# Performance work log

Measured on AMD Instinct MI355X. Metric: run time of the kernel, lower is better.

Reference implementation:

```python
import jax, jax.numpy as jnp
import numpy as np

D = 512      # d_model
H = 8        # n_head
L = 6        # n_layers
DFF = 2048   # d_inner
V = 10000    # vocab
NPOS = 2048
B, T = 8, 1023
S = 1024     # encoder length


def sinusoid_table(n_position, d_hid):
    pos = np.arange(n_position)[:, None].astype(np.float64)
    i = np.arange(d_hid)[None, :]
    angle = pos / np.power(10000.0, 2 * (i // 2) / d_hid)
    tab = np.zeros((n_position, d_hid))
    tab[:, 0::2] = np.sin(angle[:, 0::2])
    tab[:, 1::2] = np.cos(angle[:, 1::2])
    return jnp.asarray(tab, jnp.float32)


def layer_norm(x, g, b, eps=1e-6):
    m = x.mean(-1, keepdims=True)
    v = x.var(-1, keepdims=True)
    return (x - m) / jnp.sqrt(v + eps) * g + b


def mha(x, kv, wq, wk, wv, wo, g, b, mask):
    # x: [B,Lq,D], kv: [B,Lk,D], mask: [B,Lq|1,Lk] int or None
    Bq, Lq, _ = x.shape
    Lk = kv.shape[1]
    dk = D // H
    q = (x @ wq).reshape(Bq, Lq, H, dk).transpose(0, 2, 1, 3)   # bhqd
    k = (kv @ wk).reshape(Bq, Lk, H, dk).transpose(0, 2, 1, 3)  # bhkd
    v = (kv @ wv).reshape(Bq, Lk, H, dk).transpose(0, 2, 1, 3)
    scores = jnp.einsum('bhqd,bhkd->bhqk', q, k) / jnp.sqrt(jnp.asarray(dk, x.dtype))
    if mask is not None:
        scores = jnp.where(mask[:, None, :, :] == 0, jnp.asarray(-1e9, x.dtype), scores)
    a = jax.nn.softmax(scores, axis=-1)
    o = jnp.einsum('bhqk,bhkd->bhqd', a, v).transpose(0, 2, 1, 3).reshape(Bq, Lq, D)
    o = o @ wo + x  # residual
    return layer_norm(o, g, b)


def ffn(x, w1, b1, w2, b2, g, b):
    h = jax.nn.relu(x @ w1 + b1)
    return layer_norm(h @ w2 + b2 + x, g, b)


def setup_inputs() -> dict:
    key = jax.random.key(0)
    ks = iter(jax.random.split(key, 64))
    sc = 0.02
    inp = {}
    inp['trg_seq'] = jax.random.randint(next(ks), (B, T), 0, V, dtype=jnp.int32)
    # causal mask over decoder length T+1 (1 = attend)
    T1 = T + 1
    inp['trg_mask'] = jnp.tril(jnp.ones((T1, T1), jnp.int32))[None].repeat(B, axis=0)
    inp['enc_output'] = jax.random.normal(next(ks), (B, S, D), jnp.float32)
    inp['src_mask'] = jnp.ones((B, 1, S), jnp.int32)
    inp['emb'] = jax.random.normal(next(ks), (V, D), jnp.float32) * sc
    inp['ln0_g'] = jnp.ones((D,), jnp.float32)
    inp['ln0_b'] = jnp.zeros((D,), jnp.float32)
    for nm in ['wq_s', 'wk_s', 'wv_s', 'wo_s', 'wq_c', 'wk_c', 'wv_c', 'wo_c']:
        inp[nm] = jax.random.normal(next(ks), (L, D, D), jnp.float32) * sc
    for nm in ['ln1_g', 'ln2_g', 'ln3_g']:
        inp[nm] = jnp.ones((L, D), jnp.float32)
    for nm in ['ln1_b', 'ln2_b', 'ln3_b']:
        inp[nm] = jnp.zeros((L, D), jnp.float32)
    inp['w1'] = jax.random.normal(next(ks), (L, D, DFF), jnp.float32) * sc
    inp['b1'] = jnp.zeros((L, DFF), jnp.float32)
    inp['w2'] = jax.random.normal(next(ks), (L, DFF, D), jnp.float32) * sc
    inp['b2'] = jnp.zeros((L, D), jnp.float32)
    return inp


def reference(trg_seq, trg_mask, enc_output, src_mask, emb, ln0_g, ln0_b,
              wq_s, wk_s, wv_s, wo_s, ln1_g, ln1_b,
              wq_c, wk_c, wv_c, wo_c, ln2_g, ln2_b,
              w1, b1, w2, b2, ln3_g, ln3_b):
    Bq, Tq = trg_seq.shape
    tok = emb[trg_seq]                                         # [B,T,D]
    x = jnp.concatenate([jnp.zeros((Bq, 1, D), tok.dtype), tok], axis=1)  # [B,T+1,D]
    x = x + sinusoid_table(NPOS, D)[None, :Tq + 1]
    x = layer_norm(x, ln0_g, ln0_b)
    for l in range(L):
        x = mha(x, x, wq_s[l], wk_s[l], wv_s[l], wo_s[l], ln1_g[l], ln1_b[l], trg_mask)
        x = mha(x, enc_output, wq_c[l], wk_c[l], wv_c[l], wo_c[l], ln2_g[l], ln2_b[l], src_mask)
        x = ffn(x, w1[l], b1[l], w2[l], b2[l], ln3_g[l], ln3_b[l])
    return x
```

## Files before the change

kernel.cpp:

```cpp
#include <hip/hip_runtime.h>
#include <stdint.h>


typedef unsigned short u16;
typedef float floatx4 __attribute__((ext_vector_type(4)));
typedef short short8 __attribute__((ext_vector_type(8)));

__device__ __forceinline__ float b2f(u16 u) {
    union { unsigned int i; float f; } c; c.i = ((unsigned int)u) << 16; return c.f;
}
__device__ __forceinline__ u16 f2b(float f) {
    union { float f; unsigned int i; } c; c.f = f;
    return (u16)((c.i + 0x7FFFu + ((c.i >> 16) & 1u)) >> 16);
}
__device__ __forceinline__ float ldf(const void* p, size_t i, bool is32) {
    return is32 ? ((const float*)p)[i] : b2f(((const u16*)p)[i]);
}
__device__ __forceinline__ void async16(u16* lds, const u16* g) {
    __builtin_amdgcn_global_load_lds(
        (const __attribute__((address_space(1))) unsigned int*)g,
        (__attribute__((address_space(3))) unsigned int*)lds, 16, 0, 0);
}
__device__ __forceinline__ void xcd_remap(int gx, int gy, int& bx, int& by) {
    const int fid = bx + gx * by;
    const int xcd = fid & 7;
    const int i = fid >> 3;
    bx = i % gx;
    by = xcd * (gy >> 3) + i / gx;
}

__global__ __launch_bounds__(256)
void conv_bf16_kernel(const void* __restrict__ src, u16* __restrict__ dst,
                      const u16* __restrict__ probe)
{
    const bool is32 = (probe[0] == 0);
    const size_t off = ((size_t)blockIdx.x * 256 + threadIdx.x) * 4;
    u16 o[4];
    if (is32) {
        float4 f = *(const float4*)((const float*)src + off);
        o[0] = f2b(f.x); o[1] = f2b(f.y); o[2] = f2b(f.z); o[3] = f2b(f.w);
    } else {
        uint2 vv = *(const uint2*)((const u16*)src + off);
        const u16* pv = (const u16*)&vv;
        o[0] = pv[0]; o[1] = pv[1]; o[2] = pv[2]; o[3] = pv[3];
    }
    *(uint2*)&dst[off] = *(uint2*)o;
}

__global__ __launch_bounds__(256)
void transpose_layer_kernel(const void* __restrict__ wq_s, const void* __restrict__ wk_s,
                            const void* __restrict__ wv_s, const void* __restrict__ wo_s,
                            const void* __restrict__ wq_c, const void* __restrict__ wk_c,
                            const void* __restrict__ wv_c, const void* __restrict__ wo_c,
                            const void* __restrict__ w1,   const void* __restrict__ w2,
                            u16* __restrict__ wT, const u16* __restrict__ probe,
                            size_t loff2, size_t loff1)
{
    __shared__ u16 tile[32][33];
    const bool is32 = (probe[0] == 0);
    const int bid = blockIdx.x;
    const int tid = threadIdx.x;
    const void* src; u16* dst; int C, R, tr, tc; size_t loff;
    if (bid < 2048) {
        const int mat = bid >> 8, t = bid & 255;
        R = 512; C = 512; tr = t >> 4; tc = t & 15; loff = loff2;
        const void* tbl[8] = {wq_s, wk_s, wv_s, wo_s, wq_c, wk_c, wv_c, wo_c};
        src = tbl[mat]; dst = wT + (size_t)mat * 262144;
    } else if (bid < 3072) {
        const int t = bid - 2048;
        R = 512; C = 2048; tr = t >> 6; tc = t & 63; loff = loff1;
        src = w1; dst = wT + 2097152;
    } else {
        const int t = bid - 3072;
        R = 2048; C = 512; tr = t >> 4; tc = t & 15; loff = loff1;
        src = w2; dst = wT + 3145728;
    }
    const int r = tid >> 3, c0 = (tid & 7) * 4;
    const size_t off = loff + (size_t)(tr * 32 + r) * C + tc * 32 + c0;
    u16 vals[4];
    if (is32) {
        float4 f = *(const float4*)((const float*)src + off);
        vals[0] = f2b(f.x); vals[1] = f2b(f.y); vals[2] = f2b(f.z); vals[3] = f2b(f.w);
    } else {
        uint2 vv = *(const uint2*)((const u16*)src + off);
        const u16* pv = (const u16*)&vv;
        vals[0] = pv[0]; vals[1] = pv[1]; vals[2] = pv[2]; vals[3] = pv[3];
    }
#pragma unroll
    for (int j = 0; j < 4; j++) tile[r][c0 + j] = vals[j];
    __syncthreads();
    uint2 ov; u16* po = (u16*)&ov;
#pragma unroll
    for (int j = 0; j < 4; j++) po[j] = tile[c0 + j][r];
    *(uint2*)&dst[(size_t)(tc * 32 + r) * R + tr * 32 + c0] = ov;
}

template<int EPI>
__global__ __launch_bounds__(512)
void gemm256(const u16* __restrict__ A, const u16* __restrict__ Bt,
             const void* __restrict__ bias, size_t boff,
             u16* __restrict__ outb, u16* __restrict__ out1, u16* __restrict__ out2,
             const u16* __restrict__ probe, int M, int N, int K)
{
    __shared__ u16 As[2][256 * 64];
    __shared__ u16 Bs[2][256 * 64];
    const int tid = threadIdx.x;
    const int lane = tid & 63;
    const int quad = lane >> 4, cl = lane & 15;
    const int wave = tid >> 6;
    const int wm2 = (wave >> 2) * 128;
    const int wn2 = (wave & 3) * 64;
    int bx = blockIdx.x, by = blockIdx.y;
    xcd_remap(gridDim.x, gridDim.y, bx, by);
    const int m0 = by * 256, n0 = bx * 256;

    floatx4 acc[8][4];
#pragma unroll
    for (int i = 0; i < 8; i++)
#pragma unroll
        for (int j = 0; j < 4; j++)
#pragma unroll
            for (int r = 0; r < 4; r++) acc[i][j][r] = 0.0f;

    const int lrow = lane >> 3;
    const int lcol = ((lane & 7) ^ lrow) * 8;
    const u16* gA = &A [(size_t)(m0 + wave * 8 + lrow) * K + lcol];
    const u16* gB = &Bt[(size_t)(n0 + wave * 8 + lrow) * K + lcol];

    auto stage = [&](int bsel, int k0) {
#pragma unroll
        for (int s = 0; s < 4; s++)
            async16(&As[bsel][(s * 64 + wave * 8) * 64], gA + (size_t)s * 64 * K + k0);
#pragma unroll
        for (int s = 0; s < 4; s++)
            async16(&Bs[bsel][(s * 64 + wave * 8) * 64], gB + (size_t)s * 64 * K + k0);
    };

    const int nkt = K >> 6;
    stage(0, 0);
    stage(1, 64);

    const int c7 = cl & 7;
    for (int t = 0; t < nkt; ++t) {
        const int cur = t & 1;
        if (t == nkt - 1) asm volatile("s_waitcnt vmcnt(0)" ::: "memory");
        else              asm volatile("s_waitcnt vmcnt(8)" ::: "memory");
        __builtin_amdgcn_sched_barrier(0);
        __builtin_amdgcn_s_barrier();

        const u16* Ac = As[cur];
        const u16* Bc = Bs[cur];
#pragma unroll
        for (int kk = 0; kk < 2; kk++) {
            const int gsw = ((kk * 4 + quad) ^ c7) * 8;
            short8 af[8], bf[4];
#pragma unroll
            for (int mi = 0; mi < 8; mi++)
                af[mi] = *(const short8*)&Ac[(wm2 + mi * 16 + cl) * 64 + gsw];
#pragma unroll
            for (int ni = 0; ni < 4; ni++)
                bf[ni] = *(const short8*)&Bc[(wn2 + ni * 16 + cl) * 64 + gsw];
#pragma unroll
            for (int mi = 0; mi < 8; mi++)
#pragma unroll
                for (int ni = 0; ni < 4; ni++)
                    acc[mi][ni] = __builtin_amdgcn_mfma_f32_16x16x32_bf16(af[mi], bf[ni], acc[mi][ni], 0, 0, 0);
        }
        __builtin_amdgcn_s_barrier();
        __builtin_amdgcn_sched_barrier(0);
        if (t + 2 < nkt) stage(cur, (t + 2) * 64);
    }

    const bool is32 = (probe[0] == 0);
#pragma unroll
    for (int mi = 0; mi < 8; mi++) {
#pragma unroll
        for (int ni = 0; ni < 4; ni++) {
            const int col = n0 + wn2 + ni * 16 + cl;
            const float bv = ldf(bias, boff + col, is32);
#pragma unroll
            for (int r = 0; r < 4; r++) {
                const int row = m0 + wm2 + mi * 16 + quad * 4 + r;
                float v = acc[mi][ni][r] + bv;
                v = fmaxf(v, 0.0f);
                outb[(size_t)row * N + col] = f2b(v);
            }
        }
    }
}

template<int EPI>
__global__ __launch_bounds__(256)
void gemm_bf16(const u16* __restrict__ A, const u16* __restrict__ Bt,
               const void* __restrict__ bias, size_t boff, float* __restrict__ resid,
               u16* __restrict__ outb, u16* __restrict__ out1, u16* __restrict__ out2,
               const u16* __restrict__ probe, int M, int N, int K)
{
    __shared__ u16 As[3][128 * 32];
    __shared__ u16 Bs[3][128 * 32];
    const int tid = threadIdx.x;
    const int lane = tid & 63;
    const int quad = lane >> 4, cl = lane & 15;
    const int wave = tid >> 6;
    const int wm = (wave >> 1) * 64, wn = (wave & 1) * 64;
    int bx = blockIdx.x, by = blockIdx.y;
    xcd_remap(gridDim.x, gridDim.y, bx, by);
    const int m0 = by * 128, n0 = bx * 128;

    const u16* Ause = A;
    if (EPI == 4) {
        const u16* A2 = (const u16*)bias;
        if (A2 != nullptr && n0 >= 512) Ause = A2;
    }

    floatx4 acc[4][4];
#pragma unroll
    for (int i = 0; i < 4; i++)
#pragma unroll
        for (int j = 0; j < 4; j++)
#pragma unroll
            for (int r = 0; r < 4; r++) acc[i][j][r] = 0.0f;

    const int srow = tid >> 2;
    const int scol = (((tid & 3) ^ ((srow >> 1) & 3))) * 8;
    const int rslot = (quad ^ ((cl >> 1) & 3)) * 8;
    const int Ksub = K / gridDim.z;
    const int kbeg = blockIdx.z * Ksub, kend = kbeg + Ksub;
    const int nsteps = (kend - kbeg) >> 5;

    const u16* ga0 = &Ause[(size_t)(m0 + srow) * K + scol];
    const u16* ga1 = &Ause[(size_t)(m0 + 64 + srow) * K + scol];
    const u16* gb0 = &Bt[(size_t)(n0 + srow) * K + scol];
    const u16* gb1 = &Bt[(size_t)(n0 + 64 + srow) * K + scol];

    auto stage = [&](int bsel, int kk) {
        async16(&As[bsel][wave * 512],        ga0 + kk);
        async16(&As[bsel][2048 + wave * 512], ga1 + kk);
        async16(&Bs[bsel][wave * 512],        gb0 + kk);
        async16(&Bs[bsel][2048 + wave * 512], gb1 + kk);
    };

    stage(0, kbeg);
    if (nsteps > 1) stage(1, kbeg + 32);

    for (int t = 0; t < nsteps; ++t) {
        const int cur = t % 3;
        if (t + 2 < nsteps) stage((t + 2) % 3, kbeg + (t + 2) * 32);
        const int rem = nsteps - 1 - t;
        if (rem >= 2)      asm volatile("s_waitcnt vmcnt(8)" ::: "memory");
        else if (rem == 1) asm volatile("s_waitcnt vmcnt(4)" ::: "memory");
        else               asm volatile("s_waitcnt vmcnt(0)" ::: "memory");
        __builtin_amdgcn_sched_barrier(0);
        __builtin_amdgcn_s_barrier();

        const u16* Ac = As[cur];
        const u16* Bc = Bs[cur];
        short8 af[4], bfr[4];
#pragma unroll
        for (int mi = 0; mi < 4; mi++) af[mi]  = *(const short8*)&Ac[(wm + mi * 16 + cl) * 32 + rslot];
#pragma unroll
        for (int ni = 0; ni < 4; ni++) bfr[ni] = *(const short8*)&Bc[(wn + ni * 16 + cl) * 32 + rslot];
#pragma unroll
        for (int mi = 0; mi < 4; mi++)
#pragma unroll
            for (int ni = 0; ni < 4; ni++)
                acc[mi][ni] = __builtin_amdgcn_mfma_f32_16x16x32_bf16(af[mi], bfr[ni], acc[mi][ni], 0, 0, 0);
        __builtin_amdgcn_s_barrier();
    }

    if (EPI == 4) {
        const int seg = n0 >> 9;
        const int cbase = (n0 & 511) + wn;
        if (seg < 2) {
            u16* dst = (seg == 0) ? outb : out1;
#pragma unroll
            for (int mi = 0; mi < 4; mi++)
#pragma unroll
                for (int ni = 0; ni < 4; ni++) {
                    const int c = cbase + ni * 16 + cl;
#pragma unroll
                    for (int r = 0; r < 4; r++)
                        dst[(size_t)(m0 + wm + mi * 16 + quad * 4 + r) * 512 + c] = f2b(acc[mi][ni][r]);
                }
        } else {
            u16* dst = out2;
#pragma unroll
            for (int mi = 0; mi < 4; mi++) {
                const int row0 = m0 + wm + mi * 16 + quad * 4;
                const int b8 = (row0 >> 10) * 8;
                const int key0 = row0 & 1023;
#pragma unroll
                for (int ni = 0; ni < 4; ni++) {
                    const int c = cbase + ni * 16 + cl;
                    u16 pk[4];
#pragma unroll
                    for (int r = 0; r < 4; r++) pk[r] = f2b(acc[mi][ni][r]);
                    const size_t vrow = (size_t)(b8 + (c >> 6)) * 64 + (c & 63);
                    *(uint2*)&dst[vrow * 1024 + key0] = *(uint2*)pk;
                }
            }
        }
        return;
    }

    bool is32 = false;
    if (EPI == 1 || EPI == 2 || EPI == 3) is32 = (probe[0] == 0);
    const bool addbias = (bias != nullptr) && (blockIdx.z == 0);
    float* pslice = (EPI == 3) ? resid + (size_t)blockIdx.z * M * N : resid;
#pragma unroll
    for (int mi = 0; mi < 4; mi++) {
#pragma unroll
        for (int ni = 0; ni < 4; ni++) {
            const int col = n0 + wn + ni * 16 + cl;
#pragma unroll
            for (int r = 0; r < 4; r++) {
                const int row = m0 + wm + mi * 16 + quad * 4 + r;
                float v = acc[mi][ni][r];
                if (EPI == 1) { v += ldf(bias, boff + col, is32); v = fmaxf(v, 0.0f); }
                if (EPI == 2) {
                    if (addbias) v += ldf(bias, boff + col, is32);
                    atomicAdd(&resid[(size_t)row * N + col], v);
                } else if (EPI == 3) {
                    if (addbias) v += ldf(bias, boff + col, is32);
                    pslice[(size_t)row * N + col] = v;
                } else {
                    outb[(size_t)row * N + col] = f2b(v);
                }
            }
        }
    }
}

template<int CAUSAL>
__global__ __launch_bounds__(512)
void attn_kernel(const u16* __restrict__ Q, const u16* __restrict__ Kb,
                 const u16* __restrict__ VT, u16* __restrict__ O)
{
    __shared__ u16 Kt[2][64][72];
    __shared__ u16 Vt[2][64][72];
    int qt = blockIdx.x, bh = blockIdx.y;
    xcd_remap(gridDim.x, gridDim.y, qt, bh);
    const int b = bh >> 3, h = bh & 7;
    const int tid = threadIdx.x;
    const int w = tid >> 6;
    const int lane = tid & 63;
    const int quad = lane >> 4, cl = lane & 15;

    const size_t qrow = (size_t)(b * 1024 + qt * 128 + w * 16 + cl) * 512 + h * 64;
    const short8 qf0 = *(const short8*)&Q[qrow + quad * 8];
    const short8 qf1 = *(const short8*)&Q[qrow + 32 + quad * 8];
    const int qg = qt * 128 + w * 16 + cl;

    float lsum = 0.0f;
    floatx4 oacc[4];
#pragma unroll
    for (int nb = 0; nb < 4; nb++)
#pragma unroll
        for (int r = 0; r < 4; r++) oacc[nb][r] = 0.0f;

    const int trow = tid >> 3, tcol = (tid & 7) * 8;
    const int tv = tid & 7;
    const int vm = (tv >> 2) * 32 + (tv & 1) * 16 + ((tv >> 1) & 1) * 4;
    const size_t kbase = (size_t)(b * 1024) * 512 + h * 64;
    const size_t vbase = (size_t)(bh * 64) * 1024;

    const int nkt = CAUSAL ? (2 * qt + 2) : 16;
    uint4 ka = *(const uint4*)&Kb[kbase + (size_t)trow * 512 + tcol];
    uint4 va = *(const uint4*)&VT[vbase + (size_t)trow * 1024 + tcol];

    for (int kt = 0; kt < nkt; kt++) {
        const int cur = kt & 1;
        asm volatile("s_waitcnt vmcnt(0)" ::: "memory");
        *(uint4*)&Kt[cur][trow][tcol]      = ka;
        *(uint2*)&Vt[cur][trow][vm]        = make_uint2(va.x, va.y);
        *(uint2*)&Vt[cur][trow][vm + 8]    = make_uint2(va.z, va.w);
        if (kt + 1 < nkt) {
            const int k1 = (kt + 1) * 64;
            ka = *(const uint4*)&Kb[kbase + (size_t)(k1 + trow) * 512 + tcol];
            va = *(const uint4*)&VT[vbase + (size_t)trow * 1024 + k1 + tcol];
        }
        asm volatile("s_waitcnt lgkmcnt(0)" ::: "memory");
        __builtin_amdgcn_sched_barrier(0);
        __builtin_amdgcn_s_barrier();
        __builtin_amdgcn_sched_barrier(0);

        const int k0 = kt * 64;
        floatx4 sacc[4];
#pragma unroll
        for (int kb2 = 0; kb2 < 4; kb2++)
#pragma unroll
            for (int r = 0; r < 4; r++) sacc[kb2][r] = 0.0f;
#pragma unroll
        for (int kb2 = 0; kb2 < 4; kb2++) {
            const short8 kf0 = *(const short8*)&Kt[cur][kb2 * 16 + cl][quad * 8];
            const short8 kf1 = *(const short8*)&Kt[cur][kb2 * 16 + cl][32 + quad * 8];
            sacc[kb2] = __builtin_amdgcn_mfma_f32_16x16x32_bf16(kf0, qf0, sacc[kb2], 0, 0, 0);
            sacc[kb2] = __builtin_amdgcn_mfma_f32_16x16x32_bf16(kf1, qf1, sacc[kb2], 0, 0, 0);
        }
        const bool need_mask = CAUSAL && (kt >= nkt - 2);
        float p[4][4];
#pragma unroll
        for (int kb2 = 0; kb2 < 4; kb2++) {
#pragma unroll
            for (int r = 0; r < 4; r++) {
                float e = __expf(sacc[kb2][r] * 0.125f);
                if (need_mask) {
                    const int key = k0 + kb2 * 16 + quad * 4 + r;
                    e = (key > qg) ? 0.0f : e;
                }
                p[kb2][r] = e;
                lsum += e;
            }
        }
        unsigned int pk[4][2];
#pragma unroll
        for (int kb2 = 0; kb2 < 4; kb2++) {
            asm("v_cvt_pk_bf16_f32 %0, %1, %2" : "=v"(pk[kb2][0]) : "v"(p[kb2][0]), "v"(p[kb2][1]));
            asm("v_cvt_pk_bf16_f32 %0, %1, %2" : "=v"(pk[kb2][1]) : "v"(p[kb2][2]), "v"(p[kb2][3]));
        }
#pragma unroll
        for (int c = 0; c < 2; c++) {
            union { short8 s8; unsigned int u[4]; } pa;
            pa.u[0] = pk[2 * c][0];     pa.u[1] = pk[2 * c][1];
            pa.u[2] = pk[2 * c + 1][0]; pa.u[3] = pk[2 * c + 1][1];
#pragma unroll
            for (int nb = 0; nb < 4; nb++) {
                const short8 vf = *(const short8*)&Vt[cur][nb * 16 + cl][c * 32 + quad * 8];
                oacc[nb] = __builtin_amdgcn_mfma_f32_16x16x32_bf16(pa.s8, vf, oacc[nb], 0, 0, 0);
            }
        }
    }
    lsum += __shfl_xor(lsum, 16, 64);
    lsum += __shfl_xor(lsum, 32, 64);
    float inv[4];
#pragma unroll
    for (int r = 0; r < 4; r++) inv[r] = 1.0f / __shfl(lsum, quad * 4 + r, 64);
#pragma unroll
    for (int nb = 0; nb < 4; nb++) {
#pragma unroll
        for (int r = 0; r < 4; r++) {
            const float v = oacc[nb][r] * inv[r];
            O[(size_t)(b * 1024 + qt * 128 + w * 16 + quad * 4 + r) * 512 + h * 64 + nb * 16 + cl] = f2b(v);
        }
    }
}

__device__ __forceinline__ float2 block_ln_512(float v0, float v1,
                                               float g0, float g1, float b0, float b1,
                                               int tid)
{
    __shared__ float red[8];
    float s = v0 + v1, sq = v0 * v0 + v1 * v1;
#pragma unroll
    for (int m = 1; m < 64; m <<= 1) { s += __shfl_xor(s, m, 64); sq += __shfl_xor(sq, m, 64); }
    const int wv = tid >> 6;
    if ((tid & 63) == 0) { red[wv * 2] = s; red[wv * 2 + 1] = sq; }
    __syncthreads();
    s  = red[0] + red[2] + red[4] + red[6];
    sq = red[1] + red[3] + red[5] + red[7];
    const float mean = s * (1.0f / 512.0f);
    const float var = sq * (1.0f / 512.0f) - mean * mean;
    const float rstd = rsqrtf(var + 1e-6f);
    return make_float2((v0 - mean) * rstd * g0 + b0, (v1 - mean) * rstd * g1 + b1);
}

__global__ __launch_bounds__(256)
void ln_kernel(float* __restrict__ xf, const void* __restrict__ g, const void* __restrict__ bb,
               size_t goff, const u16* __restrict__ probe,
               u16* __restrict__ xb, void* __restrict__ finalout,
               const float* __restrict__ p0, const float* __restrict__ p1)
{
    const bool is32 = (probe[0] == 0);
    const int row = blockIdx.x, tid = threadIdx.x;
    const int i = tid * 2;
    const size_t base = (size_t)row * 512;
    float2 v = *(const float2*)&xf[base + i];
    if (p0) {
        const float2 a = *(const float2*)&p0[base + i];
        v.x += a.x; v.y += a.y;
    }
    if (p1) {
        const float2 b = *(const float2*)&p1[base + i];
        v.x += b.x; v.y += b.y;
    }
    const float2 y = block_ln_512(v.x, v.y, ldf(g, goff + i, is32), ldf(g, goff + i + 1, is32),
                                  ldf(bb, goff + i, is32), ldf(bb, goff + i + 1, is32), tid);
    if (finalout) {
        if (is32) {
            *(float2*)&((float*)finalout)[base + i] = y;
        } else {
            u16* ob = (u16*)finalout;
            ob[base + i] = f2b(y.x); ob[base + i + 1] = f2b(y.y);
        }
    } else {
        *(float2*)&xf[base + i] = y;
        xb[base + i] = f2b(y.x); xb[base + i + 1] = f2b(y.y);
    }
}

__global__ __launch_bounds__(256)
void embed_ln_kernel(const int* __restrict__ trg_seq, const void* __restrict__ emb,
                     const void* __restrict__ g, const void* __restrict__ bb,
                     const u16* __restrict__ probe,
                     float* __restrict__ xf, u16* __restrict__ xb)
{
    const bool is32 = (probe[0] == 0);
    const int row = blockIdx.x;
    const int b = row >> 10, t = row & 1023;
    const int tid = threadIdx.x;
    const int tok = (t == 0) ? -1 : trg_seq[b * 1023 + t - 1];
    const int i = tid * 2;
    const float freq = __expf((float)i * (-9.210340371976184f / 512.0f));
    const float angle = (float)t * freq;
    float v0 = sinf(angle), v1 = cosf(angle);
    if (tok >= 0) {
        v0 += ldf(emb, (size_t)tok * 512 + i, is32);
        v1 += ldf(emb, (size_t)tok * 512 + i + 1, is32);
    }
    const float2 y = block_ln_512(v0, v1, ldf(g, i, is32), ldf(g, i + 1, is32),
                                  ldf(bb, i, is32), ldf(bb, i + 1, is32), tid);
    const size_t base = (size_t)row * 512;
    *(float2*)&xf[base + i] = y;
    xb[base + i] = f2b(y.x); xb[base + i + 1] = f2b(y.y);
}

extern "C" void kernel_launch(void* const* d_in, const int* in_sizes, int n_in,
                              void* d_out, int out_size, void* d_ws, size_t ws_size,
                              hipStream_t stream)
{
    const int* trg_seq = (const int*)d_in[0];
    const void* enc   = d_in[2];
    const void* emb   = d_in[4];
    const void* ln0_g = d_in[5];
    const void* ln0_b = d_in[6];
    const u16* probe  = (const u16*)d_in[5];

    char* ws = (char*)d_ws;
    float* xf   = (float*)(ws);
    u16*   xb   = (u16*)  (ws + (16u << 20));
    u16*   qb   = (u16*)  (ws + (24u << 20));
    u16*   kb   = (u16*)  (ws + (32u << 20));
    u16*   vt   = (u16*)  (ws + (40u << 20));
    u16*   ao   = (u16*)  (ws + (48u << 20));
    u16*   hb   = (u16*)  (ws + (24u << 20));
    u16*   wT   = (u16*)  (ws + (56u << 20));
    u16*   encb = (u16*)  (ws + (64u << 20));
    const bool bigws = ws_size >= (108ull << 20);
    float* p0 = (float*)(ws + (72u << 20));
    float* p1 = (float*)(ws + (88u << 20));
    const float* lp0 = bigws ? p0 : nullptr;
    const float* lp1 = bigws ? p1 : nullptr;

    const size_t E2 = 262144, E1 = 1048576;
    const dim3 gqkv(12, 64);
    const dim3 gffn1(8, 32);
    const dim3 gproj(4, 64);
    const dim3 gffn2(4, 64, 2);
    const dim3 gattn(8, 64);

    conv_bf16_kernel<<<4096, 256, 0, stream>>>(enc, encb, probe);
    embed_ln_kernel<<<8192, 256, 0, stream>>>(trg_seq, emb, ln0_g, ln0_b, probe, xf, xb);

    for (int l = 0; l < 6; l++) {
        transpose_layer_kernel<<<4096, 256, 0, stream>>>(
            d_in[7], d_in[8], d_in[9], d_in[10], d_in[11], d_in[12], d_in[13], d_in[14],
            d_in[21], d_in[23], wT, probe, (size_t)l * E2, (size_t)l * E1);

        gemm_bf16<4><<<gqkv, 256, 0, stream>>>(xb, wT, xb, 0, nullptr,
                                               qb, kb, vt, probe, 8192, 1536, 512);
        attn_kernel<1><<<gattn, 512, 0, stream>>>(qb, kb, vt, ao);
        if (bigws)
            gemm_bf16<3><<<gproj, 256, 0, stream>>>(ao, wT + 3 * E2, nullptr, 0, p0,
                                                    nullptr, nullptr, nullptr, probe, 8192, 512, 512);
        else
            gemm_bf16<2><<<gproj, 256, 0, stream>>>(ao, wT + 3 * E2, nullptr, 0, xf,
                                                    nullptr, nullptr, nullptr, probe, 8192, 512, 512);
        ln_kernel<<<8192, 256, 0, stream>>>(xf, d_in[15], d_in[18], (size_t)l * 512, probe, xb,
                                            nullptr, lp0, nullptr);

        gemm_bf16<4><<<gqkv, 256, 0, stream>>>(xb, wT + 4 * E2, encb, 0, nullptr,
                                               qb, kb, vt, probe, 8192, 1536, 512);
        attn_kernel<0><<<gattn, 512, 0, stream>>>(qb, kb, vt, ao);
        if (bigws)
            gemm_bf16<3><<<gproj, 256, 0, stream>>>(ao, wT + 7 * E2, nullptr, 0, p0,
                                                    nullptr, nullptr, nullptr, probe, 8192, 512, 512);
        else
            gemm_bf16<2><<<gproj, 256, 0, stream>>>(ao, wT + 7 * E2, nullptr, 0, xf,
                                                    nullptr, nullptr, nullptr, probe, 8192, 512, 512);
        ln_kernel<<<8192, 256, 0, stream>>>(xf, d_in[16], d_in[19], (size_t)l * 512, probe, xb,
                                            nullptr, lp0, nullptr);

        gemm256<1><<<gffn1, 512, 0, stream>>>(xb, wT + 2097152, d_in[22], (size_t)l * 2048,
                                              hb, nullptr, nullptr, probe, 8192, 2048, 512);
        if (bigws)
            gemm_bf16<3><<<gffn2, 256, 0, stream>>>(hb, wT + 3145728, d_in[24], (size_t)l * 512, p0,
                                                    nullptr, nullptr, nullptr, probe, 8192, 512, 2048);
        else
            gemm_bf16<2><<<gffn2, 256, 0, stream>>>(hb, wT + 3145728, d_in[24], (size_t)l * 512, xf,
                                                    nullptr, nullptr, nullptr, probe, 8192, 512, 2048);
        ln_kernel<<<8192, 256, 0, stream>>>(xf, d_in[17], d_in[20], (size_t)l * 512, probe, xb,
                                            (l == 5) ? d_out : nullptr, lp0, lp1);
    }
}
```

Measured before the change: 1.612 ms.

## Pair causal query tiles per block to balance work and share K/V loads

Each attention block now handles two 128-row query strips, tile bx and its mirror 7-bx, so every block does the same number of causal key tiles. The K/V tiles loaded into LDS are reused by both strips, and the grid is halved from 8 to 4 along x. This is meant to remove the load imbalance of the causal triangle and cut redundant K/V traffic. In exchange it doubles the accumulator registers per thread, which may lower occupancy, and leaves fewer blocks in the grid.

```diff
diff --git a/kernel.cpp b/kernel.cpp
--- a/kernel.cpp
+++ b/kernel.cpp
@@ -338,25 +338,35 @@
 {
     __shared__ u16 Kt[2][64][72];
     __shared__ u16 Vt[2][64][72];
-    int qt = blockIdx.x, bh = blockIdx.y;
-    xcd_remap(gridDim.x, gridDim.y, qt, bh);
+    int bx = blockIdx.x, bh = blockIdx.y;
+    xcd_remap(gridDim.x, gridDim.y, bx, bh);
     const int b = bh >> 3, h = bh & 7;
     const int tid = threadIdx.x;
     const int w = tid >> 6;
     const int lane = tid & 63;
     const int quad = lane >> 4, cl = lane & 15;
 
-    const size_t qrow = (size_t)(b * 1024 + qt * 128 + w * 16 + cl) * 512 + h * 64;
-    const short8 qf0 = *(const short8*)&Q[qrow + quad * 8];
-    const short8 qf1 = *(const short8*)&Q[qrow + 32 + quad * 8];
-    const int qg = qt * 128 + w * 16 + cl;
-
-    float lsum = 0.0f;
-    floatx4 oacc[4];
+    const int sA = bx;
+    const int sB = CAUSAL ? (7 - bx) : (bx + 4);
+    const int limA = CAUSAL ? (2 * bx + 2) : 16;
+    const int nkt  = CAUSAL ? (16 - 2 * bx) : 16;
+
+    const size_t qhd = (size_t)(b * 1024) * 512 + h * 64;
+    const size_t qrA = qhd + (size_t)(sA * 128 + w * 16 + cl) * 512;
+    const size_t qrB = qhd + (size_t)(sB * 128 + w * 16 + cl) * 512;
+    const short8 qfA0 = *(const short8*)&Q[qrA + quad * 8];
+    const short8 qfA1 = *(const short8*)&Q[qrA + 32 + quad * 8];
+    const short8 qfB0 = *(const short8*)&Q[qrB + quad * 8];
+    const short8 qfB1 = *(const short8*)&Q[qrB + 32 + quad * 8];
+    const int qgA = sA * 128 + w * 16 + cl;
+    const int qgB = sB * 128 + w * 16 + cl;
+
+    float lsA = 0.0f, lsB = 0.0f;
+    floatx4 oaccA[4], oaccB[4];
 #pragma unroll
     for (int nb = 0; nb < 4; nb++)
 #pragma unroll
-        for (int r = 0; r < 4; r++) oacc[nb][r] = 0.0f;
+        for (int r = 0; r < 4; r++) { oaccA[nb][r] = 0.0f; oaccB[nb][r] = 0.0f; }
 
     const int trow = tid >> 3, tcol = (tid & 7) * 8;
     const int tv = tid & 7;
@@ -364,16 +374,62 @@
     const size_t kbase = (size_t)(b * 1024) * 512 + h * 64;
     const size_t vbase = (size_t)(bh * 64) * 1024;
 
-    const int nkt = CAUSAL ? (2 * qt + 2) : 16;
+    auto strip = [&](int cur, int k0, const short8& q0, const short8& q1,
+                     int qg, float& ls, floatx4 (&oa)[4], bool msk) {
+        floatx4 sacc[4];
+#pragma unroll
+        for (int kb2 = 0; kb2 < 4; kb2++)
+#pragma unroll
+            for (int r = 0; r < 4; r++) sacc[kb2][r] = 0.0f;
+#pragma unroll
+        for (int kb2 = 0; kb2 < 4; kb2++) {
+            const short8 kf0 = *(const short8*)&Kt[cur][kb2 * 16 + cl][quad * 8];
+            const short8 kf1 = *(const short8*)&Kt[cur][kb2 * 16 + cl][32 + quad * 8];
+            sacc[kb2] = __builtin_amdgcn_mfma_f32_16x16x32_bf16(kf0, q0, sacc[kb2], 0, 0, 0);
+            sacc[kb2] = __builtin_amdgcn_mfma_f32_16x16x32_bf16(kf1, q1, sacc[kb2], 0, 0, 0);
+        }
+        float p[4][4];
+#pragma unroll
+        for (int kb2 = 0; kb2 < 4; kb2++) {
+#pragma unroll
+            for (int r = 0; r < 4; r++) {
+                float e = __expf(sacc[kb2][r] * 0.125f);
+                if (msk) {
+                    const int key = k0 + kb2 * 16 + quad * 4 + r;
+                    e = (key > qg) ? 0.0f : e;
+                }
+                p[kb2][r] = e;
+                ls += e;
+            }
+        }
+        unsigned int pk[4][2];
+#pragma unroll
+        for (int kb2 = 0; kb2 < 4; kb2++) {
+            asm("v_cvt_pk_bf16_f32 %0, %1, %2" : "=v"(pk[kb2][0]) : "v"(p[kb2][0]), "v"(p[kb2][1]));
+            asm("v_cvt_pk_bf16_f32 %0, %1, %2" : "=v"(pk[kb2][1]) : "v"(p[kb2][2]), "v"(p[kb2][3]));
+        }
+#pragma unroll
+        for (int c = 0; c < 2; c++) {
+            union { short8 s8; unsigned int u[4]; } pa;
+            pa.u[0] = pk[2 * c][0];     pa.u[1] = pk[2 * c][1];
+            pa.u[2] = pk[2 * c + 1][0]; pa.u[3] = pk[2 * c + 1][1];
+#pragma unroll
+            for (int nb = 0; nb < 4; nb++) {
+                const short8 vf = *(const short8*)&Vt[cur][nb * 16 + cl][c * 32 + quad * 8];
+                oa[nb] = __builtin_amdgcn_mfma_f32_16x16x32_bf16(pa.s8, vf, oa[nb], 0, 0, 0);
+            }
+        }
+    };
+
     uint4 ka = *(const uint4*)&Kb[kbase + (size_t)trow * 512 + tcol];
     uint4 va = *(const uint4*)&VT[vbase + (size_t)trow * 1024 + tcol];
 
     for (int kt = 0; kt < nkt; kt++) {
         const int cur = kt & 1;
         asm volatile("s_waitcnt vmcnt(0)" ::: "memory");
-        *(uint4*)&Kt[cur][trow][tcol]      = ka;
-        *(uint2*)&Vt[cur][trow][vm]        = make_uint2(va.x, va.y);
-        *(uint2*)&Vt[cur][trow][vm + 8]    = make_uint2(va.z, va.w);
+        *(uint4*)&Kt[cur][trow][tcol]   = ka;
+        *(uint2*)&Vt[cur][trow][vm]     = make_uint2(va.x, va.y);
+        *(uint2*)&Vt[cur][trow][vm + 8] = make_uint2(va.z, va.w);
         if (kt + 1 < nkt) {
             const int k1 = (kt + 1) * 64;
             ka = *(const uint4*)&Kb[kbase + (size_t)(k1 + trow) * 512 + tcol];
@@ -385,62 +441,26 @@
         __builtin_amdgcn_sched_barrier(0);
 
         const int k0 = kt * 64;
-        floatx4 sacc[4];
-#pragma unroll
-        for (int kb2 = 0; kb2 < 4; kb2++)
-#pragma unroll
-            for (int r = 0; r < 4; r++) sacc[kb2][r] = 0.0f;
-#pragma unroll
-        for (int kb2 = 0; kb2 < 4; kb2++) {
-            const short8 kf0 = *(const short8*)&Kt[cur][kb2 * 16 + cl][quad * 8];
-            const short8 kf1 = *(const short8*)&Kt[cur][kb2 * 16 + cl][32 + quad * 8];
-            sacc[kb2] = __builtin_amdgcn_mfma_f32_16x16x32_bf16(kf0, qf0, sacc[kb2], 0, 0, 0);
-            sacc[kb2] = __builtin_amdgcn_mfma_f32_16x16x32_bf16(kf1, qf1, sacc[kb2], 0, 0, 0);
-        }
-        const bool need_mask = CAUSAL && (kt >= nkt - 2);
-        float p[4][4];
-#pragma unroll
-        for (int kb2 = 0; kb2 < 4; kb2++) {
-#pragma unroll
-            for (int r = 0; r < 4; r++) {
-                float e = __expf(sacc[kb2][r] * 0.125f);
-                if (need_mask) {
-                    const int key = k0 + kb2 * 16 + quad * 4 + r;
-                    e = (key > qg) ? 0.0f : e;
-                }
-                p[kb2][r] = e;
-                lsum += e;
-            }
-        }
-        unsigned int pk[4][2];
-#pragma unroll
-        for (int kb2 = 0; kb2 < 4; kb2++) {
-            asm("v_cvt_pk_bf16_f32 %0, %1, %2" : "=v"(pk[kb2][0]) : "v"(p[kb2][0]), "v"(p[kb2][1]));
-            asm("v_cvt_pk_bf16_f32 %0, %1, %2" : "=v"(pk[kb2][1]) : "v"(p[kb2][2]), "v"(p[kb2][3]));
-        }
-#pragma unroll
-        for (int c = 0; c < 2; c++) {
-            union { short8 s8; unsigned int u[4]; } pa;
-            pa.u[0] = pk[2 * c][0];     pa.u[1] = pk[2 * c][1];
-            pa.u[2] = pk[2 * c + 1][0]; pa.u[3] = pk[2 * c + 1][1];
-#pragma unroll
-            for (int nb = 0; nb < 4; nb++) {
-                const short8 vf = *(const short8*)&Vt[cur][nb * 16 + cl][c * 32 + quad * 8];
-                oacc[nb] = __builtin_amdgcn_mfma_f32_16x16x32_bf16(pa.s8, vf, oacc[nb], 0, 0, 0);
-            }
-        }
-    }
-    lsum += __shfl_xor(lsum, 16, 64);
-    lsum += __shfl_xor(lsum, 32, 64);
-    float inv[4];
-#pragma unroll
-    for (int r = 0; r < 4; r++) inv[r] = 1.0f / __shfl(lsum, quad * 4 + r, 64);
+        strip(cur, k0, qfB0, qfB1, qgB, lsB, oaccB, CAUSAL && (kt >= nkt - 2));
+        if (kt < limA)
+            strip(cur, k0, qfA0, qfA1, qgA, lsA, oaccA, CAUSAL && (kt >= limA - 2));
+    }
+    lsA += __shfl_xor(lsA, 16, 64); lsA += __shfl_xor(lsA, 32, 64);
+    lsB += __shfl_xor(lsB, 16, 64); lsB += __shfl_xor(lsB, 32, 64);
+    float invA[4], invB[4];
+#pragma unroll
+    for (int r = 0; r < 4; r++) {
+        invA[r] = 1.0f / __shfl(lsA, quad * 4 + r, 64);
+        invB[r] = 1.0f / __shfl(lsB, quad * 4 + r, 64);
+    }
+    const size_t orA = (size_t)(b * 1024 + sA * 128 + w * 16 + quad * 4);
+    const size_t orB = (size_t)(b * 1024 + sB * 128 + w * 16 + quad * 4);
 #pragma unroll
     for (int nb = 0; nb < 4; nb++) {
 #pragma unroll
         for (int r = 0; r < 4; r++) {
-            const float v = oacc[nb][r] * inv[r];
-            O[(size_t)(b * 1024 + qt * 128 + w * 16 + quad * 4 + r) * 512 + h * 64 + nb * 16 + cl] = f2b(v);
+            O[(orA + r) * 512 + h * 64 + nb * 16 + cl] = f2b(oaccA[nb][r] * invA[r]);
+            O[(orB + r) * 512 + h * 64 + nb * 16 + cl] = f2b(oaccB[nb][r] * invB[r]);
         }
     }
 }
@@ -556,7 +576,7 @@
     const dim3 gffn1(8, 32);
     const dim3 gproj(4, 64);
     const dim3 gffn2(4, 64, 2);
-    const dim3 gattn(8, 64);
+    const dim3 gattn(4, 64);
 
     conv_bf16_kernel<<<4096, 256, 0, stream>>>(enc, encb, probe);
     embed_ln_kernel<<<8192, 256, 0, stream>>>(trg_seq, emb, ln0_g, ln0_b, probe, xf, xb);
```

Result: faster. 1.561 ms (median of 2 runs) (-3.1%).
